# Performance work log

Hardware: AMD Instinct MI355X
Metric: run time of the kernel (lower is better)

The kernel has to match this reference:

```python
import jax, jax.numpy as jnp
import numpy as np


def setup_inputs() -> dict:
    key = jax.random.key(0)
    k1, k2, k3, k4 = jax.random.split(key, 4)
    H = W = 1024
    B = 8
    image = jax.random.uniform(k1, (1, H, W), dtype=jnp.float32)
    x = jax.random.normal(k2, (B, 1, H, W), dtype=jnp.float32)
    KL_w = jax.random.normal(k3, (9, 1, 3, 3), dtype=jnp.float32) * 0.3
    KL_b = jax.random.normal(k4, (9,), dtype=jnp.float32) * 0.1
    return {"image": image, "x": x, "KL_w": KL_w, "KL_b": KL_b}


def reference(image, x, KL_w, KL_b):
    # Per-pixel 3x3 kernel prediction: Conv2d(1, 9, k=3, padding='same')
    # image: (1, H, W) -> add batch dim -> (1, 1, H, W)
    K = jax.lax.conv_general_dilated(
        image[None], KL_w, window_strides=(1, 1), padding='SAME',
        dimension_numbers=('NCHW', 'OIHW', 'NCHW'))[0]  # (9, H, W)
    K = K + KL_b[:, None, None]

    H, W = x.shape[-2], x.shape[-1]
    xpad = jnp.pad(x, ((0, 0), (0, 0), (1, 1), (1, 1)))  # (B, C, H+2, W+2)

    # y[b,c,h,w] = sum_{a,d} xpad[b,c,h+a,w+d] * K[3a+d,h,w]
    y = jnp.zeros_like(x)
    for a in range(3):
        for d in range(3):
            y = y + xpad[..., a:a + H, d:d + W] * K[3 * a + d]
    return y
```

## Files before the change

kernel.cpp:

```cpp
#include <hip/hip_runtime.h>


#define H  1024
#define W  1024
#define NB 8
#define TD 32
#define TP 34
#define LS 36
#define LT (TP * LS)

__global__ __launch_bounds__(256)
void smblock_kernel(const float* __restrict__ image,
                    const float* __restrict__ x,
                    const float* __restrict__ kw,
                    const float* __restrict__ kb,
                    float* __restrict__ y)
{
    __shared__ float simg[LT];
    __shared__ float sx[2][LT];

    const int h0  = blockIdx.y * TD;
    const int w0  = blockIdx.x * TD;
    const int tid = threadIdx.x;
    const int r   = tid >> 3;
    const int cg  = tid & 7;

    const size_t gint = (size_t)(h0 + r) * W + (w0 + 4 * cg);
    const int    lint = (r + 1) * LS + (4 * cg + 1);

    int hr = -1, hc = -1;
    {
        const int wv = tid >> 6, ln = tid & 63;
        if      (wv == 0) { if (ln < TP) { hr = 0;      hc = ln;     } }
        else if (wv == 1) { if (ln < TP) { hr = TP - 1; hc = ln;     } }
        else if (wv == 2) { if (ln < TD) { hr = ln + 1; hc = 0;      } }
        else              { if (ln < TD) { hr = ln + 1; hc = TP - 1; } }
    }
    const bool has_halo = (hr >= 0);
    const int  gh = h0 + hr - 1, gw = w0 + hc - 1;
    const bool hin = has_halo && ((unsigned)gh < H) && ((unsigned)gw < W);
    const size_t ghalo = (size_t)gh * W + gw;
    const int    lhalo = hr * LS + hc;

    {
        float4 iv = *(const float4*)(image + gint);
        float4 xv = *(const float4*)(x + gint);
        float ihv = hin ? image[ghalo] : 0.f;
        float xhv = hin ? x[ghalo]     : 0.f;
        simg[lint]  = iv.x; simg[lint+1]  = iv.y; simg[lint+2]  = iv.z; simg[lint+3]  = iv.w;
        sx[0][lint] = xv.x; sx[0][lint+1] = xv.y; sx[0][lint+2] = xv.z; sx[0][lint+3] = xv.w;
        if (has_halo) { simg[lhalo] = ihv; sx[0][lhalo] = xhv; }
    }
    __syncthreads();

    float K[4][9];
    #pragma unroll
    for (int j = 0; j < 4; ++j)
        #pragma unroll
        for (int t = 0; t < 9; ++t) K[j][t] = kb[t];

    #pragma unroll
    for (int a = 0; a < 3; ++a) {
        const float* row = &simg[(r + a) * LS + 4 * cg];
        float4 f4 = *(const float4*)row;
        float2 f2 = *(const float2*)(row + 4);
        float wv[6] = { f4.x, f4.y, f4.z, f4.w, f2.x, f2.y };
        #pragma unroll
        for (int d = 0; d < 3; ++d)
            #pragma unroll
            for (int t = 0; t < 9; ++t) {
                float wgt = kw[t * 9 + 3 * a + d];
                #pragma unroll
                for (int j = 0; j < 4; ++j)
                    K[j][t] += wgt * wv[j + d];
            }
    }

    #pragma unroll
    for (int b = 0; b < NB; ++b) {
        float4 pv; float phv = 0.f;
        if (b + 1 < NB) {
            const float* xn = x + (size_t)(b + 1) * ((size_t)H * W);
            pv  = *(const float4*)(xn + gint);
            if (hin) phv = xn[ghalo];
        }

        const float* sb = sx[b & 1];
        float a0 = 0.f, a1 = 0.f, a2 = 0.f, a3 = 0.f;
        #pragma unroll
        for (int a = 0; a < 3; ++a) {
            const float* row = &sb[(r + a) * LS + 4 * cg];
            float4 f4 = *(const float4*)row;
            float2 f2 = *(const float2*)(row + 4);
            float wv[6] = { f4.x, f4.y, f4.z, f4.w, f2.x, f2.y };
            #pragma unroll
            for (int d = 0; d < 3; ++d) {
                a0 += wv[0 + d] * K[0][3 * a + d];
                a1 += wv[1 + d] * K[1][3 * a + d];
                a2 += wv[2 + d] * K[2][3 * a + d];
                a3 += wv[3 + d] * K[3][3 * a + d];
            }
        }
        float4 o; o.x = a0; o.y = a1; o.z = a2; o.w = a3;
        *(float4*)(y + (size_t)b * ((size_t)H * W) + gint) = o;

        if (b + 1 < NB) {
            float* dst = sx[(b + 1) & 1];
            dst[lint]   = pv.x; dst[lint+1] = pv.y;
            dst[lint+2] = pv.z; dst[lint+3] = pv.w;
            if (has_halo) dst[lhalo] = phv;
            __syncthreads();
        }
    }
}

extern "C" void kernel_launch(void* const* d_in, const int* in_sizes, int n_in,
                              void* d_out, int out_size, void* d_ws, size_t ws_size,
                              hipStream_t stream)
{
    const float* image = (const float*)d_in[0];
    const float* x     = (const float*)d_in[1];
    const float* kw    = (const float*)d_in[2];
    const float* kb    = (const float*)d_in[3];
    float* y = (float*)d_out;

    dim3 grid(W / TD, H / TD);
    smblock_kernel<<<grid, 256, 0, stream>>>(image, x, kw, kb, y);
}
```

Measured before the change: 100.1 us.

## Drop shared-memory tiling, read halos from cache, split batch across grid z

Removes the LDS tiles, double buffering and barriers, and has each thread load its 3x3 neighbourhood straight from global memory, relying on L1/L2 to serve the overlapping rows. The batch of 8 is split across two grid-z slices to double the block count, and launch bounds now ask for 4 blocks per CU. In exchange, the per-pixel kernel weights are computed twice (once per z slice), and global and cache traffic goes up from redundant halo and row reads.

```diff
diff --git a/kernel.cpp b/kernel.cpp
--- a/kernel.cpp
+++ b/kernel.cpp
@@ -5,94 +5,75 @@
 #define W  1024
 #define NB 8
 #define TD 32
-#define TP 34
-#define LS 36
-#define LT (TP * LS)
+#define SPLIT 2
+#define BPB (NB / SPLIT)
 
-__global__ __launch_bounds__(256)
+__global__ __launch_bounds__(256, 4)
 void smblock_kernel(const float* __restrict__ image,
                     const float* __restrict__ x,
                     const float* __restrict__ kw,
                     const float* __restrict__ kb,
                     float* __restrict__ y)
 {
-    __shared__ float simg[LT];
-    __shared__ float sx[2][LT];
-
-    const int h0  = blockIdx.y * TD;
-    const int w0  = blockIdx.x * TD;
     const int tid = threadIdx.x;
     const int r   = tid >> 3;
     const int cg  = tid & 7;
-
-    const size_t gint = (size_t)(h0 + r) * W + (w0 + 4 * cg);
-    const int    lint = (r + 1) * LS + (4 * cg + 1);
-
-    int hr = -1, hc = -1;
-    {
-        const int wv = tid >> 6, ln = tid & 63;
-        if      (wv == 0) { if (ln < TP) { hr = 0;      hc = ln;     } }
-        else if (wv == 1) { if (ln < TP) { hr = TP - 1; hc = ln;     } }
-        else if (wv == 2) { if (ln < TD) { hr = ln + 1; hc = 0;      } }
-        else              { if (ln < TD) { hr = ln + 1; hc = TP - 1; } }
-    }
-    const bool has_halo = (hr >= 0);
-    const int  gh = h0 + hr - 1, gw = w0 + hc - 1;
-    const bool hin = has_halo && ((unsigned)gh < H) && ((unsigned)gw < W);
-    const size_t ghalo = (size_t)gh * W + gw;
-    const int    lhalo = hr * LS + hc;
-
-    {
-        float4 iv = *(const float4*)(image + gint);
-        float4 xv = *(const float4*)(x + gint);
-        float ihv = hin ? image[ghalo] : 0.f;
-        float xhv = hin ? x[ghalo]     : 0.f;
-        simg[lint]  = iv.x; simg[lint+1]  = iv.y; simg[lint+2]  = iv.z; simg[lint+3]  = iv.w;
-        sx[0][lint] = xv.x; sx[0][lint+1] = xv.y; sx[0][lint+2] = xv.z; sx[0][lint+3] = xv.w;
-        if (has_halo) { simg[lhalo] = ihv; sx[0][lhalo] = xhv; }
-    }
-    __syncthreads();
+    const int h0  = blockIdx.y * TD;
+    const int w0  = blockIdx.x * TD;
+    const int gw  = w0 + 4 * cg;
+    const int gh0 = h0 + r;
+    const bool lok = (gw > 0);
+    const bool rok = (gw + 4 < W);
 
     float K[4][9];
     #pragma unroll
-    for (int j = 0; j < 4; ++j)
-        #pragma unroll
-        for (int t = 0; t < 9; ++t) K[j][t] = kb[t];
+    for (int t = 0; t < 9; ++t) {
+        const float bt = kb[t];
+        K[0][t] = bt; K[1][t] = bt; K[2][t] = bt; K[3][t] = bt;
+    }
 
     #pragma unroll
     for (int a = 0; a < 3; ++a) {
-        const float* row = &simg[(r + a) * LS + 4 * cg];
-        float4 f4 = *(const float4*)row;
-        float2 f2 = *(const float2*)(row + 4);
-        float wv[6] = { f4.x, f4.y, f4.z, f4.w, f2.x, f2.y };
+        const int gh = gh0 + a - 1;
+        float wv[6] = {0.f, 0.f, 0.f, 0.f, 0.f, 0.f};
+        if ((unsigned)gh < H) {
+            const float* p = image + (size_t)gh * W + gw;
+            float4 m = *(const float4*)p;
+            wv[1] = m.x; wv[2] = m.y; wv[3] = m.z; wv[4] = m.w;
+            if (lok) wv[0] = p[-1];
+            if (rok) wv[5] = p[4];
+        }
         #pragma unroll
-        for (int d = 0; d < 3; ++d)
+        for (int d = 0; d < 3; ++d) {
             #pragma unroll
             for (int t = 0; t < 9; ++t) {
-                float wgt = kw[t * 9 + 3 * a + d];
+                const float wgt = kw[t * 9 + 3 * a + d];
                 #pragma unroll
                 for (int j = 0; j < 4; ++j)
                     K[j][t] += wgt * wv[j + d];
             }
+        }
     }
 
+    const int    b0  = blockIdx.z * BPB;
+    const size_t pix = (size_t)gh0 * W + gw;
+
     #pragma unroll
-    for (int b = 0; b < NB; ++b) {
-        float4 pv; float phv = 0.f;
-        if (b + 1 < NB) {
-            const float* xn = x + (size_t)(b + 1) * ((size_t)H * W);
-            pv  = *(const float4*)(xn + gint);
-            if (hin) phv = xn[ghalo];
-        }
+    for (int bi = 0; bi < BPB; ++bi) {
+        const float* xb = x + (size_t)(b0 + bi) * ((size_t)H * W);
+        float a0 = 0.f, a1 = 0.f, a2 = 0.f, a3 = 0.f;
 
-        const float* sb = sx[b & 1];
-        float a0 = 0.f, a1 = 0.f, a2 = 0.f, a3 = 0.f;
         #pragma unroll
         for (int a = 0; a < 3; ++a) {
-            const float* row = &sb[(r + a) * LS + 4 * cg];
-            float4 f4 = *(const float4*)row;
-            float2 f2 = *(const float2*)(row + 4);
-            float wv[6] = { f4.x, f4.y, f4.z, f4.w, f2.x, f2.y };
+            const int gh = gh0 + a - 1;
+            float wv[6] = {0.f, 0.f, 0.f, 0.f, 0.f, 0.f};
+            if ((unsigned)gh < H) {
+                const float* p = xb + (size_t)gh * W + gw;
+                float4 m = *(const float4*)p;
+                wv[1] = m.x; wv[2] = m.y; wv[3] = m.z; wv[4] = m.w;
+                if (lok) wv[0] = p[-1];
+                if (rok) wv[5] = p[4];
+            }
             #pragma unroll
             for (int d = 0; d < 3; ++d) {
                 a0 += wv[0 + d] * K[0][3 * a + d];
@@ -102,15 +83,7 @@
             }
         }
         float4 o; o.x = a0; o.y = a1; o.z = a2; o.w = a3;
-        *(float4*)(y + (size_t)b * ((size_t)H * W) + gint) = o;
-
-        if (b + 1 < NB) {
-            float* dst = sx[(b + 1) & 1];
-            dst[lint]   = pv.x; dst[lint+1] = pv.y;
-            dst[lint+2] = pv.z; dst[lint+3] = pv.w;
-            if (has_halo) dst[lhalo] = phv;
-            __syncthreads();
-        }
+        *(float4*)(y + (size_t)(b0 + bi) * ((size_t)H * W) + pix) = o;
     }
 }
 
@@ -124,6 +97,6 @@
     const float* kb    = (const float*)d_in[3];
     float* y = (float*)d_out;
 
-    dim3 grid(W / TD, H / TD);
+    dim3 grid(W / TD, H / TD, SPLIT);
     smblock_kernel<<<grid, 256, 0, stream>>>(image, x, kw, kb, y);
 }
```

Measured after the change: 106.7 us. 6.6% more time.
